# Performance work log

Measured on AMD Instinct MI355X. Metric: run time of the kernel, lower is better.

Reference implementation:

```python
import jax, jax.numpy as jnp
import numpy as np

IMG = 1024       # original image resolution implied by (1024 - 1) normalization
STRIDE = 16
TEMP = 0.1
EPS = 1e-12      # F.normalize eps


def setup_inputs() -> dict:
    key = jax.random.key(0)
    k1, k2, k3, k4, k5 = jax.random.split(key, 5)
    B, C, Hf, Wf, N = 32, 256, 64, 64, 128
    feats_src = jax.random.normal(k1, (B, C, Hf, Wf), dtype=jnp.float32)
    feats_trg = jax.random.normal(k2, (B, C, Hf, Wf), dtype=jnp.float32)
    kps_src = jax.random.uniform(k3, (B, N, 2), dtype=jnp.float32) * (IMG - 1)
    kps_trg = jax.random.uniform(k4, (B, N, 2), dtype=jnp.float32) * (IMG - 1)
    kps_mask = jax.random.randint(k5, (B, N), 0, 2, dtype=jnp.int32)
    return {"feats_src": feats_src, "feats_trg": feats_trg,
            "kps_src": kps_src, "kps_trg": kps_trg, "kps_mask": kps_mask}


def _l2norm_c(x):
    # F.normalize(x, dim=1): x / max(||x||_2, eps) along channel dim
    n = jnp.sqrt(jnp.sum(x * x, axis=1, keepdims=True))
    return x / jnp.maximum(n, EPS)


def _bilinear_sample(feats, kps):
    # feats: [B,C,Hf,Wf]; kps: [B,N,2] pixel coords in [0, IMG-1]
    # Equivalent to F.grid_sample(align_corners=True, bilinear) with
    # grid = kps/(IMG-1)*2-1 -> pixel coords kps/(IMG-1)*(size-1).
    B, C, Hf, Wf = feats.shape
    x = kps[..., 0] / (IMG - 1) * (Wf - 1)  # [B,N]
    y = kps[..., 1] / (IMG - 1) * (Hf - 1)
    x0 = jnp.clip(jnp.floor(x), 0, Wf - 1).astype(jnp.int32)
    y0 = jnp.clip(jnp.floor(y), 0, Hf - 1).astype(jnp.int32)
    x1 = jnp.clip(x0 + 1, 0, Wf - 1)
    y1 = jnp.clip(y0 + 1, 0, Hf - 1)
    fx = x - x0.astype(x.dtype)
    fy = y - y0.astype(y.dtype)
    ft = jnp.transpose(feats, (0, 2, 3, 1))      # [B,Hf,Wf,C]
    bb = jnp.arange(B)[:, None]                  # [B,1] broadcasts to [B,N]
    g = lambda yy, xx: ft[bb, yy, xx]            # [B,N,C]
    wa = ((1 - fx) * (1 - fy))[..., None]
    wb = ((1 - fx) * fy)[..., None]
    wc = (fx * (1 - fy))[..., None]
    wd = (fx * fy)[..., None]
    return wa * g(y0, x0) + wb * g(y1, x0) + wc * g(y0, x1) + wd * g(y1, x1)


def reference(feats_src, feats_trg, kps_src, kps_trg, kps_mask):
    B, C, Hf, Wf = feats_src.shape
    N = kps_src.shape[1]
    fs = _l2norm_c(feats_src)
    ftg = _l2norm_c(feats_trg)

    # Query features sampled at source keypoints: [B,N,C]
    q = _bilinear_sample(fs, kps_src)

    # Logits over all target spatial positions: [B,N,Hf*Wf]
    trg_flat = ftg.reshape(B, C, Hf * Wf)
    logits = jnp.einsum('bnc,bcm->bnm', q, trg_flat) / TEMP

    # Bilinear soft targets at target keypoints (feature-grid coords)
    gx = kps_trg[..., 0] / STRIDE
    gy = kps_trg[..., 1] / STRIDE
    x0 = jnp.clip(jnp.floor(gx), 0, Wf - 1).astype(jnp.int32)
    x1 = jnp.clip(x0 + 1, 0, Wf - 1)
    y0 = jnp.clip(jnp.floor(gy), 0, Hf - 1).astype(jnp.int32)
    y1 = jnp.clip(y0 + 1, 0, Hf - 1)
    x0f, x1f = x0.astype(gx.dtype), x1.astype(gx.dtype)
    y0f, y1f = y0.astype(gy.dtype), y1.astype(gy.dtype)
    wa = (x1f - gx) * (y1f - gy)
    wb = (x1f - gx) * (gy - y0f)
    wc = (gx - x0f) * (y1f - gy)
    wd = (gx - x0f) * (gy - y0f)

    m = (kps_mask != 0).astype(logits.dtype)     # [B,N]
    w = jnp.stack([wa, wb, wc, wd], axis=-1) * m[..., None]   # [B,N,4]
    idx = jnp.stack([y0 * Wf + x0, y1 * Wf + x0,
                     y0 * Wf + x1, y1 * Wf + x1], axis=-1)    # [B,N,4]
    bb = jnp.arange(B)[:, None, None]
    nn = jnp.arange(N)[None, :, None]
    soft_targets = jnp.zeros_like(logits).at[bb, nn, idx].add(w)

    log_probs = jax.nn.log_softmax(logits, axis=-1)
    loss = -(soft_targets * log_probs).sum(axis=-1)           # [B,N]
    denom = jnp.maximum(m.sum(), 1.0)
    return (loss * m).sum() / denom
```

## Files before the change

kernel.cpp:

```cpp
#include <hip/hip_runtime.h>
#include <math.h>

#define B_    32
#define C_    256
#define HF    64
#define WF    64
#define M_    4096
#define N_    128
#define IMGM1 1023.0f
#define TEMP_ 0.1f
#define EPS_  1e-12f
#define NCH   32
#define SAS   40

typedef __attribute__((ext_vector_type(8))) short short8;
typedef __attribute__((ext_vector_type(4))) float floatx4;

__device__ __forceinline__ unsigned short f2bf(float x) {
  unsigned int u = __float_as_uint(x);
  u += 0x7fffu + ((u >> 16) & 1u);
  return (unsigned short)(u >> 16);
}
__device__ __forceinline__ float bf2f(unsigned short h) {
  return __uint_as_float(((unsigned int)h) << 16);
}
__device__ __forceinline__ float wave_sum(float v) {
#pragma unroll
  for (int off = 32; off; off >>= 1) v += __shfl_down(v, off, 64);
  return v;
}

__device__ __forceinline__ void src_geom(float kx, float ky, int& x0, int& y0,
                                         int& x1, int& y1, float& fx, float& fy) {
  const float x = kx / IMGM1 * (float)(WF - 1);
  const float y = ky / IMGM1 * (float)(HF - 1);
  x0 = (int)fminf(fmaxf(floorf(x), 0.f), 63.f);
  y0 = (int)fminf(fmaxf(floorf(y), 0.f), 63.f);
  x1 = min(x0 + 1, 63);
  y1 = min(y0 + 1, 63);
  fx = x - (float)x0;
  fy = y - (float)y0;
}

__global__ __launch_bounds__(256) void k1a_stage(const float* __restrict__ fs,
                                                 const float* __restrict__ kps,
                                                 ushort* __restrict__ corner,
                                                 float* __restrict__ ssqg) {
  const int cg = blockIdx.x, b = blockIdx.y, t = threadIdx.x;
  const int c0 = cg * 2;
  __shared__ __align__(16) float plane[2 * M_];
  __shared__ float4 ssq2[256];

  const float4* src = (const float4*)(fs + ((size_t)(b * C_ + c0)) * M_);
  float4* dst = (float4*)plane;
#pragma unroll
  for (int i = 0; i < 8; i++) dst[t + 256 * i] = src[t + 256 * i];
  __syncthreads();

  const int n = t & 127, p = t >> 7;
  const int c = c0 + p;
  const float kx = kps[((size_t)b * N_ + n) * 2 + 0];
  const float ky = kps[((size_t)b * N_ + n) * 2 + 1];
  int x0, y0, x1, y1; float fx, fy;
  src_geom(kx, ky, x0, y0, x1, y1, fx, fy);

  const float* pl = plane + p * M_;
  const float f00 = pl[y0 * WF + x0];
  const float f10 = pl[y1 * WF + x0];
  const float f01 = pl[y0 * WF + x1];
  const float f11 = pl[y1 * WF + x1];

  ushort4 cr;
  cr.x = f2bf(f00); cr.y = f2bf(f10); cr.z = f2bf(f01); cr.w = f2bf(f11);
  *(ushort4*)&corner[(((size_t)b * C_ + c) * N_ + n) * 4] = cr;

  ssq2[t] = make_float4(f00 * f00, f10 * f10, f01 * f01, f11 * f11);
  __syncthreads();
  if (t < 128) {
    const float4 a = ssq2[t], bq = ssq2[t + 128];
    float* g = ssqg + ((size_t)b * N_ + t) * 4;
    atomicAdd(g + 0, a.x + bq.x);
    atomicAdd(g + 1, a.y + bq.y);
    atomicAdd(g + 2, a.z + bq.z);
    atomicAdd(g + 3, a.w + bq.w);
  }
}

__global__ __launch_bounds__(256) void k1b2_combine(const ushort* __restrict__ corner,
                                                    const float* __restrict__ ssqg,
                                                    const float* __restrict__ kps,
                                                    ushort* __restrict__ qbf) {
  const int cg = blockIdx.x, b = blockIdx.y, t = threadIdx.x;
  __shared__ float4 uw[128];
  __shared__ ushort sQ[32][137];

  if (t < 128) {
    const int n = t;
    const float kx = kps[((size_t)b * N_ + n) * 2 + 0];
    const float ky = kps[((size_t)b * N_ + n) * 2 + 1];
    int x0, y0, x1, y1; float fx, fy;
    src_geom(kx, ky, x0, y0, x1, y1, fx, fy);
    const float wa = (1.f - fx) * (1.f - fy), wb = (1.f - fx) * fy;
    const float wc = fx * (1.f - fy), wd = fx * fy;
    const float4 sq = *(const float4*)&ssqg[((size_t)b * N_ + n) * 4];
    const float r0 = 1.f / fmaxf(sqrtf(sq.x), EPS_);
    const float r1 = 1.f / fmaxf(sqrtf(sq.y), EPS_);
    const float r2 = 1.f / fmaxf(sqrtf(sq.z), EPS_);
    const float r3 = 1.f / fmaxf(sqrtf(sq.w), EPS_);
    uw[n] = make_float4(wa * r0, wb * r1, wc * r2, wd * r3);
  }
  __syncthreads();

  const ushort* cb = corner + (((size_t)b * C_ + cg * 32) * N_) * 4;
#pragma unroll
  for (int i = 0; i < 16; i++) {
    const int e = t + 256 * i;
    const int n = e & 127, cl = e >> 7;
    const ushort4 cr = *(const ushort4*)&cb[((size_t)cl * N_ + n) * 4];
    const float4 u = uw[n];
    const float qv = u.x * bf2f(cr.x) + u.y * bf2f(cr.y) +
                     u.z * bf2f(cr.z) + u.w * bf2f(cr.w);
    sQ[cl][n] = f2bf(qv);
  }
  __syncthreads();

  ushort* qb = qbf + (size_t)b * N_ * C_ + cg * 32;
#pragma unroll
  for (int i = 0; i < 4; i++) {
    const int o = t + 256 * i;
    const int n = o >> 3, c4 = (o & 7) * 4;
    ushort4 w4;
    w4.x = sQ[c4 + 0][n]; w4.y = sQ[c4 + 1][n];
    w4.z = sQ[c4 + 2][n]; w4.w = sQ[c4 + 3][n];
    *(ushort4*)&qb[(size_t)n * C_ + c4] = w4;
  }
}

__global__ __launch_bounds__(256) void k2_mfma(const float* __restrict__ trg,
                                               const ushort* __restrict__ qbf,
                                               const float* __restrict__ kps_trg,
                                               const int* __restrict__ mask,
                                               float2* __restrict__ part,
                                               float* __restrict__ tacc) {
  const int t = threadIdx.x;
  const int mb = blockIdx.x, b = blockIdx.y;
  const int m0 = mb * 128;
  const int wave = t >> 6, lane = t & 63;
  const int wn = wave >> 1, wm = wave & 1;
  const int lg = lane >> 4, ln = lane & 15;

  __shared__ __align__(16) short sA[128 * SAS];
  __shared__ __align__(16) short sB[128 * SAS];
  __shared__ __align__(16) float ssqp[16 * 128];
  __shared__ float scl[128];
  __shared__ float2 lser[128 * 2];
  __shared__ __align__(16) int   tidx[128][4];
  __shared__ __align__(16) float tw[128][4];
  __shared__ unsigned tmask[128];

  floatx4 acc[4][4];
#pragma unroll
  for (int i = 0; i < 4; i++)
#pragma unroll
    for (int j = 0; j < 4; j++) acc[i][j] = (floatx4)0.f;

  float ssq[8];
#pragma unroll
  for (int e = 0; e < 8; e++) ssq[e] = 0.f;

  const ushort* qb = qbf + (size_t)b * N_ * C_;
  const float*  tb = trg + (size_t)b * C_ * M_ + m0;
  const int kk  = 2 * (t >> 4);
  const int m8  = (t & 15) * 8;
  const int gB  = kk >> 3;
  const int kin = kk & 7;

  for (int k0 = 0; k0 < C_; k0 += 32) {
#pragma unroll
    for (int l2 = 0; l2 < 2; l2++) {
      const int flat = t + 256 * l2;
      const int an = flat >> 2, ag = flat & 3;
      const short8 v = *(const short8*)(qb + an * C_ + k0 + ag * 8);
      *(short8*)&sA[an * SAS + ag * 8] = v;
    }
    {
      const float* p0 = tb + (size_t)(k0 + kk) * M_ + m8;
      const float* p1 = p0 + M_;
      const float4 a0 = *(const float4*)p0, a1 = *(const float4*)(p0 + 4);
      const float4 b0 = *(const float4*)p1, b1 = *(const float4*)(p1 + 4);
      const float v0[8] = {a0.x, a0.y, a0.z, a0.w, a1.x, a1.y, a1.z, a1.w};
      const float v1[8] = {b0.x, b0.y, b0.z, b0.w, b1.x, b1.y, b1.z, b1.w};
#pragma unroll
      for (int e = 0; e < 8; e++) {
        ssq[e] += v0[e] * v0[e] + v1[e] * v1[e];
        const int m = m8 + e;
        const int fm = (m >> 3) & 3;
        const unsigned int pr = (unsigned int)f2bf(v0[e]) | ((unsigned int)f2bf(v1[e]) << 16);
        *(unsigned int*)&sB[m * SAS + ((gB ^ fm) << 3) + kin] = pr;
      }
    }
    __syncthreads();
    short8 af[4], bfr[4];
#pragma unroll
    for (int i = 0; i < 4; i++)
      af[i] = *(const short8*)&sA[(wn * 64 + i * 16 + ln) * SAS + (lg << 3)];
#pragma unroll
    for (int j = 0; j < 4; j++) {
      const int m = wm * 64 + j * 16 + ln;
      const int fm = (m >> 3) & 3;
      bfr[j] = *(const short8*)&sB[m * SAS + ((lg ^ fm) << 3)];
    }
#pragma unroll
    for (int i = 0; i < 4; i++)
#pragma unroll
      for (int j = 0; j < 4; j++)
        acc[i][j] = __builtin_amdgcn_mfma_f32_16x16x32_bf16(af[i], bfr[j], acc[i][j], 0, 0, 0);
    __syncthreads();
  }

  *(float4*)&ssqp[(t >> 4) * 128 + m8]     = make_float4(ssq[0], ssq[1], ssq[2], ssq[3]);
  *(float4*)&ssqp[(t >> 4) * 128 + m8 + 4] = make_float4(ssq[4], ssq[5], ssq[6], ssq[7]);
  __syncthreads();
  if (t < 128) {
    float s = 0.f;
#pragma unroll
    for (int g = 0; g < 16; g++) s += ssqp[g * 128 + t];
    scl[t] = 1.f / (fmaxf(sqrtf(s), EPS_) * TEMP_);
    const float kx = kps_trg[((size_t)b * N_ + t) * 2 + 0];
    const float ky = kps_trg[((size_t)b * N_ + t) * 2 + 1];
    const float gx = kx * (1.f / 16.f), gy = ky * (1.f / 16.f);
    const int x0 = (int)fminf(fmaxf(floorf(gx), 0.f), 63.f);
    const int y0 = (int)fminf(fmaxf(floorf(gy), 0.f), 63.f);
    const int x1 = min(x0 + 1, 63), y1 = min(y0 + 1, 63);
    const float x0f = (float)x0, x1f = (float)x1, y0f = (float)y0, y1f = (float)y1;
    const float mk = (mask[(size_t)b * N_ + t] != 0) ? 1.f : 0.f;
    const int i0 = y0 * WF + x0, i1 = y1 * WF + x0;
    const int i2 = y0 * WF + x1, i3 = y1 * WF + x1;
    const float w0 = (x1f - gx) * (y1f - gy) * mk;
    const float w1 = (x1f - gx) * (gy - y0f) * mk;
    const float w2 = (gx - x0f) * (y1f - gy) * mk;
    const float w3 = (gx - x0f) * (gy - y0f) * mk;
    tidx[t][0] = i0; tw[t][0] = w0;
    tidx[t][1] = i1; tw[t][1] = w1;
    tidx[t][2] = i2; tw[t][2] = w2;
    tidx[t][3] = i3; tw[t][3] = w3;
    unsigned tm = 0u;
    if (w0 != 0.f) tm |= 1u << (i0 >> 7);
    if (w1 != 0.f) tm |= 1u << (i1 >> 7);
    if (w2 != 0.f) tm |= 1u << (i2 >> 7);
    if (w3 != 0.f) tm |= 1u << (i3 >> 7);
    tmask[t] = tm;
  }
  __syncthreads();

  float scj[4];
#pragma unroll
  for (int j = 0; j < 4; j++) scj[j] = scl[wm * 64 + j * 16 + ln];
#pragma unroll
  for (int i = 0; i < 4; i++)
#pragma unroll
    for (int j = 0; j < 4; j++) acc[i][j] *= scj[j];

  const unsigned mbbit = 1u << mb;
#pragma unroll
  for (int i = 0; i < 4; i++) {
#pragma unroll
    for (int r = 0; r < 4; r++) {
      float mx = fmaxf(fmaxf(acc[i][0][r], acc[i][1][r]), fmaxf(acc[i][2][r], acc[i][3][r]));
#pragma unroll
      for (int msk = 1; msk < 16; msk <<= 1) mx = fmaxf(mx, __shfl_xor(mx, msk, 64));
      float sm = __expf(acc[i][0][r] - mx) + __expf(acc[i][1][r] - mx) +
                 __expf(acc[i][2][r] - mx) + __expf(acc[i][3][r] - mx);
#pragma unroll
      for (int msk = 1; msk < 16; msk <<= 1) sm += __shfl_xor(sm, msk, 64);
      if (ln == 0) lser[(wn * 64 + i * 16 + lg * 4 + r) * 2 + wm] = make_float2(mx, sm);

      const int n = wn * 64 + i * 16 + lg * 4 + r;
      if (tmask[n] & mbbit) {
        const int4  id4 = *(const int4*)&tidx[n][0];
        const float4 w4 = *(const float4*)&tw[n][0];
        const int   ida[4] = {id4.x, id4.y, id4.z, id4.w};
        const float wwa[4] = {w4.x, w4.y, w4.z, w4.w};
#pragma unroll
        for (int j = 0; j < 4; j++) {
          const int mg = m0 + wm * 64 + j * 16 + ln;
          const float lv = acc[i][j][r];
#pragma unroll
          for (int cc = 0; cc < 4; cc++)
            if (ida[cc] == mg && wwa[cc] != 0.f)
              atomicAdd(&tacc[(size_t)b * N_ + n], wwa[cc] * lv);
        }
      }
    }
  }
  __syncthreads();
  if (t < 128) {
    const float2 u = lser[t * 2 + 0], v = lser[t * 2 + 1];
    const float M = fmaxf(u.x, v.x);
    const float S = u.y * __expf(u.x - M) + v.y * __expf(v.x - M);
    part[((size_t)b * N_ + t) * NCH + mb] = make_float2(M, S);
  }
}

__global__ __launch_bounds__(128) void k4_comb(const float2* __restrict__ part,
                                               const float* __restrict__ tacc,
                                               const float* __restrict__ kps_trg,
                                               const int* __restrict__ mask,
                                               float* __restrict__ gs) {
  const int b = blockIdx.x, t = threadIdx.x;
  const float2* p = part + ((size_t)b * N_ + t) * NCH;
  float M = -INFINITY;
#pragma unroll 8
  for (int c = 0; c < NCH; c++) M = fmaxf(M, p[c].x);
  float S = 0.f;
#pragma unroll 8
  for (int c = 0; c < NCH; c++) S += p[c].y * __expf(p[c].x - M);
  const float lse = M + logf(S);

  const float kx = kps_trg[((size_t)b * N_ + t) * 2 + 0];
  const float ky = kps_trg[((size_t)b * N_ + t) * 2 + 1];
  const float gx = kx * (1.f / 16.f), gy = ky * (1.f / 16.f);
  const int x0 = (int)fminf(fmaxf(floorf(gx), 0.f), 63.f);
  const int y0 = (int)fminf(fmaxf(floorf(gy), 0.f), 63.f);
  const int x1 = min(x0 + 1, 63), y1 = min(y0 + 1, 63);
  const float mk = (mask[(size_t)b * N_ + t] != 0) ? 1.f : 0.f;
  const float wsum = (float)(x1 - x0) * (float)(y1 - y0) * mk;

  float loss = wsum * lse - tacc[(size_t)b * N_ + t];
  float cnt = mk;
  loss = wave_sum(loss);
  cnt = wave_sum(cnt);
  __shared__ float sl[2], sc2[2];
  if ((t & 63) == 0) { sl[t >> 6] = loss; sc2[t >> 6] = cnt; }
  __syncthreads();
  if (t == 0) {
    atomicAdd(&gs[0], sl[0] + sl[1]);
    atomicAdd(&gs[1], sc2[0] + sc2[1]);
  }
}

__global__ void k5_final(const float* __restrict__ gs, float* __restrict__ out) {
  out[0] = gs[0] / fmaxf(gs[1], 1.f);
}

extern "C" void kernel_launch(void* const* d_in, const int* in_sizes, int n_in,
                              void* d_out, int out_size, void* d_ws, size_t ws_size,
                              hipStream_t stream) {
  const float* feats_src = (const float*)d_in[0];
  const float* feats_trg = (const float*)d_in[1];
  const float* kps_src   = (const float*)d_in[2];
  const float* kps_trg   = (const float*)d_in[3];
  const int*   kps_mask  = (const int*)d_in[4];
  float* out = (float*)d_out;

  char* wsb = (char*)d_ws;
  float*  ssqg   = (float*)(wsb + 0);
  float*  tacc   = (float*)(wsb + 65536);
  float*  gs     = (float*)(wsb + 81920);
  ushort* corner = (ushort*)(wsb + 82432);
  ushort* qbf    = (ushort*)(wsb + 8471040);
  float2* part   = (float2*)(wsb + 10568192);

  hipMemsetAsync(wsb, 0, 81928, stream);

  k1a_stage<<<dim3(C_ / 2, B_), 256, 0, stream>>>(feats_src, kps_src, corner, ssqg);
  k1b2_combine<<<dim3(C_ / 32, B_), 256, 0, stream>>>(corner, ssqg, kps_src, qbf);
  k2_mfma<<<dim3(NCH, B_), 256, 0, stream>>>(feats_trg, qbf, kps_trg, kps_mask, part, tacc);
  k4_comb<<<dim3(B_), 128, 0, stream>>>(part, tacc, kps_trg, kps_mask, gs);
  k5_final<<<1, 1, 0, stream>>>(gs, out);
}
```

Baseline: 327.4 us.

## Prefetch next K-slice into registers and coalesce target loads in k2_mfma

Global loads for the next 32-channel slice of the query and target tiles are now issued into registers before the MFMA phase of the current slice, so memory latency overlaps with compute. The per-thread target column mapping changes from 8 contiguous floats to two float4 groups 64 apart, which makes a 16-thread group read a contiguous 256-byte row, and the sum-of-squares scatter is updated to match. The launch bounds also gain a min-blocks hint of 4, which caps register use and may cause spills given the extra prefetch registers.

```diff
diff --git a/kernel.cpp b/kernel.cpp
--- a/kernel.cpp
+++ b/kernel.cpp
@@ -136,12 +136,12 @@
   }
 }
 
-__global__ __launch_bounds__(256) void k2_mfma(const float* __restrict__ trg,
-                                               const ushort* __restrict__ qbf,
-                                               const float* __restrict__ kps_trg,
-                                               const int* __restrict__ mask,
-                                               float2* __restrict__ part,
-                                               float* __restrict__ tacc) {
+__global__ __launch_bounds__(256, 4) void k2_mfma(const float* __restrict__ trg,
+                                                  const ushort* __restrict__ qbf,
+                                                  const float* __restrict__ kps_trg,
+                                                  const int* __restrict__ mask,
+                                                  float2* __restrict__ part,
+                                                  float* __restrict__ tacc) {
   const int t = threadIdx.x;
   const int mb = blockIdx.x, b = blockIdx.y;
   const int m0 = mb * 128;
@@ -171,34 +171,53 @@
   const ushort* qb = qbf + (size_t)b * N_ * C_;
   const float*  tb = trg + (size_t)b * C_ * M_ + m0;
   const int kk  = 2 * (t >> 4);
-  const int m8  = (t & 15) * 8;
+  const int m4  = (t & 15) * 4;
   const int gB  = kk >> 3;
   const int kin = kk & 7;
 
+  const ushort* qA0 = qb + (t >> 2) * C_ + (t & 3) * 8;
+  const ushort* qA1 = qA0 + 64 * C_;
+  const int aoff = (t >> 2) * SAS + (t & 3) * 8;
+  const float* tbase = tb + (size_t)kk * M_ + m4;
+
+  short8 rA0, rA1;
+  float4 rBa0, rBa1, rBb0, rBb1;
+
+  rA0 = *(const short8*)(qA0);
+  rA1 = *(const short8*)(qA1);
+  {
+    const float* p0 = tbase;
+    const float* p1 = p0 + M_;
+    rBa0 = *(const float4*)p0;  rBa1 = *(const float4*)(p0 + 64);
+    rBb0 = *(const float4*)p1;  rBb1 = *(const float4*)(p1 + 64);
+  }
+
   for (int k0 = 0; k0 < C_; k0 += 32) {
-#pragma unroll
-    for (int l2 = 0; l2 < 2; l2++) {
-      const int flat = t + 256 * l2;
-      const int an = flat >> 2, ag = flat & 3;
-      const short8 v = *(const short8*)(qb + an * C_ + k0 + ag * 8);
-      *(short8*)&sA[an * SAS + ag * 8] = v;
-    }
+    *(short8*)&sA[aoff] = rA0;
+    *(short8*)&sA[aoff + 64 * SAS] = rA1;
     {
-      const float* p0 = tb + (size_t)(k0 + kk) * M_ + m8;
-      const float* p1 = p0 + M_;
-      const float4 a0 = *(const float4*)p0, a1 = *(const float4*)(p0 + 4);
-      const float4 b0 = *(const float4*)p1, b1 = *(const float4*)(p1 + 4);
-      const float v0[8] = {a0.x, a0.y, a0.z, a0.w, a1.x, a1.y, a1.z, a1.w};
-      const float v1[8] = {b0.x, b0.y, b0.z, b0.w, b1.x, b1.y, b1.z, b1.w};
+      const float v0[8] = {rBa0.x, rBa0.y, rBa0.z, rBa0.w, rBa1.x, rBa1.y, rBa1.z, rBa1.w};
+      const float v1[8] = {rBb0.x, rBb0.y, rBb0.z, rBb0.w, rBb1.x, rBb1.y, rBb1.z, rBb1.w};
 #pragma unroll
       for (int e = 0; e < 8; e++) {
         ssq[e] += v0[e] * v0[e] + v1[e] * v1[e];
-        const int m = m8 + e;
+        const int m = m4 + (e & 3) + ((e >> 2) << 6);
         const int fm = (m >> 3) & 3;
         const unsigned int pr = (unsigned int)f2bf(v0[e]) | ((unsigned int)f2bf(v1[e]) << 16);
         *(unsigned int*)&sB[m * SAS + ((gB ^ fm) << 3) + kin] = pr;
       }
     }
+    {
+      const int kn = k0 + 32;
+      if (kn < C_) {
+        rA0 = *(const short8*)(qA0 + kn);
+        rA1 = *(const short8*)(qA1 + kn);
+        const float* p0 = tbase + (size_t)kn * M_;
+        const float* p1 = p0 + M_;
+        rBa0 = *(const float4*)p0;  rBa1 = *(const float4*)(p0 + 64);
+        rBb0 = *(const float4*)p1;  rBb1 = *(const float4*)(p1 + 64);
+      }
+    }
     __syncthreads();
     short8 af[4], bfr[4];
 #pragma unroll
@@ -218,8 +237,8 @@
     __syncthreads();
   }
 
-  *(float4*)&ssqp[(t >> 4) * 128 + m8]     = make_float4(ssq[0], ssq[1], ssq[2], ssq[3]);
-  *(float4*)&ssqp[(t >> 4) * 128 + m8 + 4] = make_float4(ssq[4], ssq[5], ssq[6], ssq[7]);
+  *(float4*)&ssqp[(t >> 4) * 128 + m4]      = make_float4(ssq[0], ssq[1], ssq[2], ssq[3]);
+  *(float4*)&ssqp[(t >> 4) * 128 + m4 + 64] = make_float4(ssq[4], ssq[5], ssq[6], ssq[7]);
   __syncthreads();
   if (t < 128) {
     float s = 0.f;
```

Measured after the change: 347.5 us. 6.1% more time.

## Pre-transpose target features to bf16 and register-prefetch GEMM tiles

Applied to the files above, without the earlier changes.

Adds a separate kernel that converts feats_trg to bf16, transposes it to [B,M,C], and writes per-position partial sums of squares. The GEMM kernel then loads both operands as contiguous 16-byte bf16 vectors, prefetches the next K-slice into registers while the current one is used, and reads the norms from the precomputed buffer instead of reducing them in shared memory. This removes fp32 strided loads and in-loop conversion from the GEMM, at the cost of one extra launch plus writing and rereading a 64MB bf16 intermediate.

```diff
diff --git a/kernel.cpp b/kernel.cpp
--- a/kernel.cpp
+++ b/kernel.cpp
@@ -84,6 +84,45 @@
     atomicAdd(g + 2, a.z + bq.z);
     atomicAdd(g + 3, a.w + bq.w);
   }
+}
+
+__global__ __launch_bounds__(256) void k1c_trgT(const float* __restrict__ ft,
+                                                ushort* __restrict__ trgT,
+                                                float* __restrict__ psq) {
+  const int mblk = blockIdx.x, cblk = blockIdx.y, b = blockIdx.z;
+  const int m0 = mblk * 64, c0 = cblk * 64;
+  const int t = threadIdx.x;
+  __shared__ ushort sTT[64][66];
+  __shared__ float sp[4][64];
+
+  const int ml = t & 63, cg = t >> 6;
+  const float* src = ft + ((size_t)(b * C_ + c0 + cg * 16)) * M_ + m0 + ml;
+  float ss = 0.f;
+#pragma unroll
+  for (int g = 0; g < 4; g++) {
+    const float v0 = src[(size_t)(g * 4 + 0) * M_];
+    const float v1 = src[(size_t)(g * 4 + 1) * M_];
+    const float v2 = src[(size_t)(g * 4 + 2) * M_];
+    const float v3 = src[(size_t)(g * 4 + 3) * M_];
+    ss += v0 * v0 + v1 * v1 + v2 * v2 + v3 * v3;
+    const unsigned p0 = (unsigned)f2bf(v0) | ((unsigned)f2bf(v1) << 16);
+    const unsigned p1 = (unsigned)f2bf(v2) | ((unsigned)f2bf(v3) << 16);
+    *(unsigned*)&sTT[ml][cg * 16 + g * 4 + 0] = p0;
+    *(unsigned*)&sTT[ml][cg * 16 + g * 4 + 2] = p1;
+  }
+  sp[cg][ml] = ss;
+  __syncthreads();
+
+  if (t < 64)
+    psq[((size_t)b * 4 + cblk) * M_ + m0 + t] = sp[0][t] + sp[1][t] + sp[2][t] + sp[3][t];
+
+  const int mo = t >> 2, cc = (t & 3) * 16;
+  unsigned w[8];
+#pragma unroll
+  for (int p = 0; p < 8; p++) w[p] = *(const unsigned*)&sTT[mo][cc + 2 * p];
+  ushort* dst = trgT + ((size_t)(b * M_ + m0 + mo)) * C_ + c0 + cc;
+  *(uint4*)(dst + 0) = make_uint4(w[0], w[1], w[2], w[3]);
+  *(uint4*)(dst + 8) = make_uint4(w[4], w[5], w[6], w[7]);
 }
 
 __global__ __launch_bounds__(256) void k1b2_combine(const ushort* __restrict__ corner,
@@ -136,8 +175,9 @@
   }
 }
 
-__global__ __launch_bounds__(256) void k2_mfma(const float* __restrict__ trg,
+__global__ __launch_bounds__(256) void k2_mfma(const ushort* __restrict__ trgT,
                                                const ushort* __restrict__ qbf,
+                                               const float* __restrict__ psq,
                                                const float* __restrict__ kps_trg,
                                                const int* __restrict__ mask,
                                                float2* __restrict__ part,
@@ -151,7 +191,6 @@
 
   __shared__ __align__(16) short sA[128 * SAS];
   __shared__ __align__(16) short sB[128 * SAS];
-  __shared__ __align__(16) float ssqp[16 * 128];
   __shared__ float scl[128];
   __shared__ float2 lser[128 * 2];
   __shared__ __align__(16) int   tidx[128][4];
@@ -164,39 +203,35 @@
 #pragma unroll
     for (int j = 0; j < 4; j++) acc[i][j] = (floatx4)0.f;
 
-  float ssq[8];
-#pragma unroll
-  for (int e = 0; e < 8; e++) ssq[e] = 0.f;
-
   const ushort* qb = qbf + (size_t)b * N_ * C_;
-  const float*  tb = trg + (size_t)b * C_ * M_ + m0;
-  const int kk  = 2 * (t >> 4);
-  const int m8  = (t & 15) * 8;
-  const int gB  = kk >> 3;
-  const int kin = kk & 7;
+  const ushort* tT = trgT + ((size_t)b * M_ + m0) * C_;
+
+  const int row = t >> 2, ch = (t & 3) * 8;
+  const ushort* qA0 = qb + (size_t)row * C_ + ch;
+  const ushort* qA1 = qA0 + (size_t)64 * C_;
+  const ushort* qB0 = tT + (size_t)row * C_ + ch;
+  const ushort* qB1 = qB0 + (size_t)64 * C_;
+  const int soff = row * SAS + ch;
+
+  short8 rA0, rA1, rB0, rB1;
+
+  rA0 = *(const short8*)(qA0);
+  rA1 = *(const short8*)(qA1);
+  rB0 = *(const short8*)(qB0);
+  rB1 = *(const short8*)(qB1);
 
   for (int k0 = 0; k0 < C_; k0 += 32) {
-#pragma unroll
-    for (int l2 = 0; l2 < 2; l2++) {
-      const int flat = t + 256 * l2;
-      const int an = flat >> 2, ag = flat & 3;
-      const short8 v = *(const short8*)(qb + an * C_ + k0 + ag * 8);
-      *(short8*)&sA[an * SAS + ag * 8] = v;
-    }
+    *(short8*)&sA[soff]            = rA0;
+    *(short8*)&sA[soff + 64 * SAS] = rA1;
+    *(short8*)&sB[soff]            = rB0;
+    *(short8*)&sB[soff + 64 * SAS] = rB1;
     {
-      const float* p0 = tb + (size_t)(k0 + kk) * M_ + m8;
-      const float* p1 = p0 + M_;
-      const float4 a0 = *(const float4*)p0, a1 = *(const float4*)(p0 + 4);
-      const float4 b0 = *(const float4*)p1, b1 = *(const float4*)(p1 + 4);
-      const float v0[8] = {a0.x, a0.y, a0.z, a0.w, a1.x, a1.y, a1.z, a1.w};
-      const float v1[8] = {b0.x, b0.y, b0.z, b0.w, b1.x, b1.y, b1.z, b1.w};
-#pragma unroll
-      for (int e = 0; e < 8; e++) {
-        ssq[e] += v0[e] * v0[e] + v1[e] * v1[e];
-        const int m = m8 + e;
-        const int fm = (m >> 3) & 3;
-        const unsigned int pr = (unsigned int)f2bf(v0[e]) | ((unsigned int)f2bf(v1[e]) << 16);
-        *(unsigned int*)&sB[m * SAS + ((gB ^ fm) << 3) + kin] = pr;
+      const int kn = k0 + 32;
+      if (kn < C_) {
+        rA0 = *(const short8*)(qA0 + kn);
+        rA1 = *(const short8*)(qA1 + kn);
+        rB0 = *(const short8*)(qB0 + kn);
+        rB1 = *(const short8*)(qB1 + kn);
       }
     }
     __syncthreads();
@@ -205,11 +240,8 @@
     for (int i = 0; i < 4; i++)
       af[i] = *(const short8*)&sA[(wn * 64 + i * 16 + ln) * SAS + (lg << 3)];
 #pragma unroll
-    for (int j = 0; j < 4; j++) {
-      const int m = wm * 64 + j * 16 + ln;
-      const int fm = (m >> 3) & 3;
-      bfr[j] = *(const short8*)&sB[m * SAS + ((lg ^ fm) << 3)];
-    }
+    for (int j = 0; j < 4; j++)
+      bfr[j] = *(const short8*)&sB[(wm * 64 + j * 16 + ln) * SAS + (lg << 3)];
 #pragma unroll
     for (int i = 0; i < 4; i++)
 #pragma unroll
@@ -218,13 +250,11 @@
     __syncthreads();
   }
 
-  *(float4*)&ssqp[(t >> 4) * 128 + m8]     = make_float4(ssq[0], ssq[1], ssq[2], ssq[3]);
-  *(float4*)&ssqp[(t >> 4) * 128 + m8 + 4] = make_float4(ssq[4], ssq[5], ssq[6], ssq[7]);
-  __syncthreads();
   if (t < 128) {
-    float s = 0.f;
-#pragma unroll
-    for (int g = 0; g < 16; g++) s += ssqp[g * 128 + t];
+    const float s = psq[((size_t)b * 4 + 0) * M_ + m0 + t]
+                  + psq[((size_t)b * 4 + 1) * M_ + m0 + t]
+                  + psq[((size_t)b * 4 + 2) * M_ + m0 + t]
+                  + psq[((size_t)b * 4 + 3) * M_ + m0 + t];
     scl[t] = 1.f / (fmaxf(sqrtf(s), EPS_) * TEMP_);
     const float kx = kps_trg[((size_t)b * N_ + t) * 2 + 0];
     const float ky = kps_trg[((size_t)b * N_ + t) * 2 + 1];
@@ -360,12 +390,15 @@
   ushort* corner = (ushort*)(wsb + 82432);
   ushort* qbf    = (ushort*)(wsb + 8471040);
   float2* part   = (float2*)(wsb + 10568192);
+  float*  psq    = (float*)(wsb + 11616768);
+  ushort* trgT   = (ushort*)(wsb + 13713920);
 
   hipMemsetAsync(wsb, 0, 81928, stream);
 
   k1a_stage<<<dim3(C_ / 2, B_), 256, 0, stream>>>(feats_src, kps_src, corner, ssqg);
+  k1c_trgT<<<dim3(M_ / 64, C_ / 64, B_), 256, 0, stream>>>(feats_trg, trgT, psq);
   k1b2_combine<<<dim3(C_ / 32, B_), 256, 0, stream>>>(corner, ssqg, kps_src, qbf);
-  k2_mfma<<<dim3(NCH, B_), 256, 0, stream>>>(feats_trg, qbf, kps_trg, kps_mask, part, tacc);
+  k2_mfma<<<dim3(NCH, B_), 256, 0, stream>>>(trgT, qbf, psq, kps_trg, kps_mask, part, tacc);
   k4_comb<<<dim3(B_), 128, 0, stream>>>(part, tacc, kps_trg, kps_mask, gs);
   k5_final<<<1, 1, 0, stream>>>(gs, out);
 }
```

Result: slower. 355.5 us (+8.6%).
